# Kernel tuning notes

Measured on AMD Instinct MI355X. Metric: run time of the kernel, lower is better.

Reference implementation:

```python
import jax, jax.numpy as jnp
import numpy as np
from jax import lax

N, F, V = 16, 5, 4  # batch, frames, nodes-per-frame

def _maxpool3(x):
    # MaxPool2d(kernel=3, stride=3), NCHW
    return lax.reduce_window(x, -jnp.inf, lax.max, (1, 1, 3, 3), (1, 1, 3, 3), 'VALID')

def _conv(x, w, b):
    y = lax.conv_general_dilated(x, w, window_strides=(2, 2), padding='VALID',
                                 dimension_numbers=('NCHW', 'OIHW', 'NCHW'))
    return y + b[None, :, None, None]

def setup_inputs() -> dict:
    key = jax.random.key(0)
    ks = jax.random.split(key, 24)
    s = 0.05
    inp = {
        'nodes':  jax.random.normal(ks[0], (N, F, V, 3, 224, 224), jnp.float32),
        'pos':    jax.random.normal(ks[1], (N, F, V, 6), jnp.float32),
        'attmap': jax.random.uniform(ks[2], (N, F, V, V), jnp.float32),
        'depths': jax.random.normal(ks[3], (N, F, V), jnp.float32),
        # params (linear weights stored [in, out]; y = x @ W + b)
        'conv1_w': jax.random.normal(ks[4], (3, 3, 3, 3), jnp.float32) * s,
        'conv1_b': jax.random.normal(ks[5], (3,), jnp.float32) * s,
        'conv2_w': jax.random.normal(ks[6], (1, 3, 3, 3), jnp.float32) * s,
        'conv2_b': jax.random.normal(ks[7], (1,), jnp.float32) * s,
        'lin_w':   jax.random.normal(ks[8], (36, 6), jnp.float32) * s,
        'lin_b':   jax.random.normal(ks[9], (6,), jnp.float32) * s,
        'wfc_w':   jax.random.normal(ks[10], (24, 1), jnp.float32) * s,
        'wfc_b':   jax.random.normal(ks[11], (1,), jnp.float32) * s,
        'fm_w':    jax.random.normal(ks[12], (6, 6), jnp.float32) * s,
        'fm_b':    jax.random.normal(ks[13], (6,), jnp.float32) * s,
        'lm_w':    jax.random.normal(ks[14], (6, 6), jnp.float32) * s,
        'lm_b':    jax.random.normal(ks[15], (6,), jnp.float32) * s,
        'fc1_w':   jax.random.normal(ks[16], (240, 120), jnp.float32) * s,
        'fc1_b':   jax.random.normal(ks[17], (120,), jnp.float32) * s,
        'fc2_w':   jax.random.normal(ks[18], (120, 60), jnp.float32) * s,
        'fc2_b':   jax.random.normal(ks[19], (60,), jnp.float32) * s,
        'fc3_w':   jax.random.normal(ks[20], (60, 6), jnp.float32) * s,
        'fc3_b':   jax.random.normal(ks[21], (6,), jnp.float32) * s,
    }
    return inp

def reference(nodes, pos, attmap, depths,
              conv1_w, conv1_b, conv2_w, conv2_b, lin_w, lin_b,
              wfc_w, wfc_b, fm_w, fm_b, lm_w, lm_b,
              fc1_w, fc1_b, fc2_w, fc2_b, fc3_w, fc3_b):
    # --- CNN node encoder ---
    x = nodes.reshape(N * F * V, 3, 224, 224)
    h = jax.nn.relu(_maxpool3(_conv(x, conv1_w, conv1_b)))          # [B*,3,37,37]
    h = jax.nn.relu(_maxpool3(_conv(h, conv2_w, conv2_b)))          # [B*,1,6,6]
    feat = h.reshape(N, F, V, 36) @ lin_w + lin_b                    # [N,F,V,6]

    # --- edge weights: sigmoid(W . cat(feat_src, feat_tgt)) ---
    na = jnp.concatenate([feat, pos], axis=-1)                       # [N,F,V,12]
    src = jnp.broadcast_to(na[:, :, :, None, :], (N, F, V, V, 12))   # s along axis 2
    tgt = jnp.broadcast_to(na[:, :, None, :, :], (N, F, V, V, 12))   # t along axis 3
    ef = jnp.concatenate([src, tgt], axis=-1)                        # [N,F,V,V,24]
    link = jax.nn.sigmoid((ef @ wfc_w)[..., 0] + wfc_b[0])           # [N,F,s,t]

    maw = link + attmap                                              # [N,F,s,t]

    # --- attention-weighted message aggregation over source nodes ---
    pm = pos @ fm_w + fm_b                                           # [N,F,V,6]
    agg = jnp.einsum('bfsn,bfsd->bfnd', maw, pm)                     # [N,F,V,6]

    # last-frame message (frame 0 has none)
    prev = jnp.concatenate([jnp.zeros_like(pos[:, :1]), pos[:, :-1]], axis=1)
    lm = prev @ lm_w + lm_b                                          # [N,F,V,6]
    frame_mask = (jnp.arange(F) > 0)[None, :, None, None]
    pos_up = agg + jnp.where(frame_mask, lm, 0.0)

    # --- readout MLP ---
    inp = jnp.concatenate([feat, pos_up], axis=-1).reshape(N, F * V * 12)  # [N,240]
    r = jax.nn.relu(inp @ fc1_w + fc1_b)
    r = jax.nn.relu(r @ fc2_w + fc2_b)
    return r @ fc3_w + fc3_b                                         # [N,6]
```

## Files before the change

### kernel.cpp

```cpp
#include <hip/hip_runtime.h>
#include <math.h>

#define NB 16
#define NF 5
#define NV 4
#define NIMG (NB*NF*NV)
#define IMG_HW 224
#define IMG_CH_STRIDE (224*224)
#define H1_HW 37
#define H1_CH_STRIDE (37*37)
#define H1_IMG 4108

__global__ __launch_bounds__(256) void k1_conv1_pool(
    const float* __restrict__ nodes,
    const float* __restrict__ w,
    const float* __restrict__ bias,
    float* __restrict__ h1)
{
    const int blk = blockIdx.x;
    const int img = blk / H1_HW;
    const int py  = blk - img * H1_HW;
    const int t   = threadIdx.x;

    __shared__ float s[3 * 7 * 224];

    const float* src = nodes + (size_t)img * 3 * IMG_CH_STRIDE + py * 6 * IMG_HW;

    {
        const float4* s0 = (const float4*)(src);
        const float4* s1 = (const float4*)(src + IMG_CH_STRIDE);
        const float4* s2 = (const float4*)(src + 2 * IMG_CH_STRIDE);
        float4* d0 = (float4*)s;
        float4* d1 = (float4*)(s + 1568);
        float4* d2 = (float4*)(s + 3136);
        const bool hi = (t < 392 - 256);
        float4 a0 = s0[t], a1 = s1[t], a2 = s2[t];
        float4 b0, b1, b2;
        if (hi) { b0 = s0[t + 256]; b1 = s1[t + 256]; b2 = s2[t + 256]; }
        d0[t] = a0; d1[t] = a1; d2[t] = a2;
        if (hi) { d0[t + 256] = b0; d1[t + 256] = b1; d2[t + 256] = b2; }
    }
    __syncthreads();

    if (t < H1_HW) {
        const int px = t;
        float acc[3][9];
        #pragma unroll
        for (int oc = 0; oc < 3; ++oc)
            #pragma unroll
            for (int p = 0; p < 9; ++p) acc[oc][p] = 0.f;

        #pragma unroll
        for (int ic = 0; ic < 3; ++ic) {
            float wv[3][3][3];
            #pragma unroll
            for (int oc = 0; oc < 3; ++oc)
                #pragma unroll
                for (int ky = 0; ky < 3; ++ky)
                    #pragma unroll
                    for (int kx = 0; kx < 3; ++kx)
                        wv[oc][ky][kx] = w[((oc * 3 + ic) * 3 + ky) * 3 + kx];

            float patch[7][8];
            #pragma unroll
            for (int r = 0; r < 7; ++r) {
                const float* row = s + ic * 1568 + r * 224 + 6 * px;
                #pragma unroll
                for (int k = 0; k < 4; ++k) {
                    float2 q = *(const float2*)(row + 2 * k);
                    patch[r][2 * k]     = q.x;
                    patch[r][2 * k + 1] = q.y;
                }
            }

            #pragma unroll
            for (int i = 0; i < 3; ++i)
                #pragma unroll
                for (int j = 0; j < 3; ++j) {
                    const int p = i * 3 + j;
                    #pragma unroll
                    for (int ky = 0; ky < 3; ++ky)
                        #pragma unroll
                        for (int kx = 0; kx < 3; ++kx) {
                            float x = patch[2 * i + ky][2 * j + kx];
                            acc[0][p] += wv[0][ky][kx] * x;
                            acc[1][p] += wv[1][ky][kx] * x;
                            acc[2][p] += wv[2][ky][kx] * x;
                        }
                }
        }

        float* outb = h1 + (size_t)img * H1_IMG + py * H1_HW + px;
        #pragma unroll
        for (int oc = 0; oc < 3; ++oc) {
            float m = -INFINITY;
            #pragma unroll
            for (int p = 0; p < 9; ++p) m = fmaxf(m, acc[oc][p]);
            m += bias[oc];
            m = fmaxf(m, 0.f);
            outb[oc * H1_CH_STRIDE] = m;
        }
    }
}

__global__ __launch_bounds__(128) void k2_conv2_pool_lin(
    const float* __restrict__ h1,
    const float* __restrict__ w2,
    const float* __restrict__ b2,
    const float* __restrict__ lin_w,
    const float* __restrict__ lin_b,
    float* __restrict__ feat)
{
    const int img = blockIdx.x;
    const int t   = threadIdx.x;
    __shared__ float s[H1_IMG];
    __shared__ float s_h2[36];

    {
        const float4* src = (const float4*)(h1 + (size_t)img * H1_IMG);
        float4* d = (float4*)s;
        float4 v[8];
        #pragma unroll
        for (int k = 0; k < 8; ++k) v[k] = src[t + 128 * k];
        const bool hi = (t < 1027 - 1024);
        float4 v8;
        if (hi) v8 = src[t + 1024];
        #pragma unroll
        for (int k = 0; k < 8; ++k) d[t + 128 * k] = v[k];
        if (hi) d[t + 1024] = v8;
    }
    __syncthreads();

    if (t < 36) {
        const int py = t / 6, px = t - (t / 6) * 6;
        float m = -INFINITY;
        #pragma unroll
        for (int i = 0; i < 3; ++i)
            #pragma unroll
            for (int j = 0; j < 3; ++j) {
                const int oy = 3 * py + i, ox = 3 * px + j;
                float a = 0.f;
                #pragma unroll
                for (int ic = 0; ic < 3; ++ic)
                    #pragma unroll
                    for (int ky = 0; ky < 3; ++ky)
                        #pragma unroll
                        for (int kx = 0; kx < 3; ++kx)
                            a += w2[(ic * 3 + ky) * 3 + kx] *
                                 s[ic * H1_CH_STRIDE + (2 * oy + ky) * H1_HW + (2 * ox + kx)];
                m = fmaxf(m, a);
            }
        m += b2[0];
        s_h2[t] = fmaxf(m, 0.f);
    }
    __syncthreads();
    if (t < 6) {
        float a = lin_b[t];
        #pragma unroll
        for (int i = 0; i < 36; ++i) a += s_h2[i] * lin_w[i * 6 + t];
        feat[img * 6 + t] = a;
    }
}

__global__ __launch_bounds__(128) void k3_graph_mlp(
    const float* __restrict__ feat,
    const float* __restrict__ pos,
    const float* __restrict__ attmap,
    const float* __restrict__ wfc_w,
    const float* __restrict__ wfc_b,
    const float* __restrict__ fm_w,
    const float* __restrict__ fm_b,
    const float* __restrict__ lm_w,
    const float* __restrict__ lm_b,
    const float* __restrict__ fc1_w,
    const float* __restrict__ fc1_b,
    const float* __restrict__ fc2_w,
    const float* __restrict__ fc2_b,
    const float* __restrict__ fc3_w,
    const float* __restrict__ fc3_b,
    float* __restrict__ out)
{
    const int b = blockIdx.x;
    const int t = threadIdx.x;

    __shared__ float s_na[NF][NV][12];
    __shared__ float s_pm[NF][NV][6];
    __shared__ float s_maw[NF][NV][NV];
    __shared__ float s_inp[240];
    __shared__ float s_r1[120];
    __shared__ float s_r2[60];

    if (t < 120) {
        int f = t / 24;
        int v = (t / 6) % 4;
        int d = t % 6;
        float fv = feat[((b * NF + f) * NV + v) * 6 + d];
        float pv = pos[((b * NF + f) * NV + v) * 6 + d];
        s_na[f][v][d]     = fv;
        s_na[f][v][6 + d] = pv;
        s_inp[(f * NV + v) * 12 + d] = fv;
    }
    __syncthreads();

    if (t < 120) {
        int f = t / 24;
        int v = (t / 6) % 4;
        int d = t % 6;
        float a = fm_b[d];
        #pragma unroll
        for (int k = 0; k < 6; ++k) a += s_na[f][v][6 + k] * fm_w[k * 6 + d];
        s_pm[f][v][d] = a;
    }
    if (t < 80) {
        int f = t / 16;
        int sidx = (t / 4) % 4;
        int tt = t % 4;
        float x = wfc_b[0];
        #pragma unroll
        for (int k = 0; k < 12; ++k)
            x += wfc_w[k] * s_na[f][sidx][k] + wfc_w[12 + k] * s_na[f][tt][k];
        float sig = 1.f / (1.f + expf(-x));
        s_maw[f][sidx][tt] = sig + attmap[((b * NF + f) * NV + sidx) * NV + tt];
    }
    __syncthreads();

    if (t < 120) {
        int f = t / 24;
        int n = (t / 6) % 4;
        int d = t % 6;
        float a = 0.f;
        #pragma unroll
        for (int sidx = 0; sidx < 4; ++sidx) a += s_maw[f][sidx][n] * s_pm[f][sidx][d];
        if (f > 0) {
            float l = lm_b[d];
            #pragma unroll
            for (int k = 0; k < 6; ++k) l += s_na[f - 1][n][6 + k] * lm_w[k * 6 + d];
            a += l;
        }
        s_inp[(f * NV + n) * 12 + 6 + d] = a;
    }
    __syncthreads();

    if (t < 120) {
        float a = fc1_b[t];
        #pragma unroll 16
        for (int i = 0; i < 240; ++i) a += s_inp[i] * fc1_w[i * 120 + t];
        s_r1[t] = fmaxf(a, 0.f);
    }
    __syncthreads();

    if (t < 60) {
        float a = fc2_b[t];
        #pragma unroll 16
        for (int i = 0; i < 120; ++i) a += s_r1[i] * fc2_w[i * 60 + t];
        s_r2[t] = fmaxf(a, 0.f);
    }
    __syncthreads();

    if (t < 6) {
        float a = fc3_b[t];
        #pragma unroll 12
        for (int i = 0; i < 60; ++i) a += s_r2[i] * fc3_w[i * 6 + t];
        out[b * 6 + t] = a;
    }
}

extern "C" void kernel_launch(void* const* d_in, const int* in_sizes, int n_in,
                              void* d_out, int out_size, void* d_ws, size_t ws_size,
                              hipStream_t stream) {
    const float* nodes   = (const float*)d_in[0];
    const float* pos     = (const float*)d_in[1];
    const float* attmap  = (const float*)d_in[2];
    const float* conv1_w = (const float*)d_in[4];
    const float* conv1_b = (const float*)d_in[5];
    const float* conv2_w = (const float*)d_in[6];
    const float* conv2_b = (const float*)d_in[7];
    const float* lin_w   = (const float*)d_in[8];
    const float* lin_b   = (const float*)d_in[9];
    const float* wfc_w   = (const float*)d_in[10];
    const float* wfc_b   = (const float*)d_in[11];
    const float* fm_w    = (const float*)d_in[12];
    const float* fm_b    = (const float*)d_in[13];
    const float* lm_w    = (const float*)d_in[14];
    const float* lm_b    = (const float*)d_in[15];
    const float* fc1_w   = (const float*)d_in[16];
    const float* fc1_b   = (const float*)d_in[17];
    const float* fc2_w   = (const float*)d_in[18];
    const float* fc2_b   = (const float*)d_in[19];
    const float* fc3_w   = (const float*)d_in[20];
    const float* fc3_b   = (const float*)d_in[21];

    float* h1      = (float*)d_ws;
    float* feat_ws = h1 + (size_t)NIMG * H1_IMG;

    k1_conv1_pool<<<NIMG * H1_HW, 256, 0, stream>>>(nodes, conv1_w, conv1_b, h1);
    k2_conv2_pool_lin<<<NIMG, 128, 0, stream>>>(h1, conv2_w, conv2_b, lin_w, lin_b, feat_ws);
    k3_graph_mlp<<<NB, 128, 0, stream>>>(feat_ws, pos, attmap,
                                         wfc_w, wfc_b, fm_w, fm_b, lm_w, lm_b,
                                         fc1_w, fc1_b, fc2_w, fc2_b, fc3_w, fc3_b,
                                         (float*)d_out);
}
```

Baseline: 328.8 us.

## Process two pooled rows per block and split output channels across threads

Each conv1+pool block now handles two pooled output rows, loading 13 input rows into shared memory instead of 7. This shares the overlapping halo row and halves the number of blocks. Work is spread so each of up to 222 threads computes one output channel for one pixel, instead of 37 threads computing all three channels, which raises active lanes per block. Weights and bias are staged in shared memory, and the input loads use nontemporal hints. In exchange the blocks use more LDS, and each patch is read from shared memory three times, once per channel thread.

After: 321.2 us (median of 2 runs). 1.02x faster.

```diff
diff --git a/kernel.cpp b/kernel.cpp
--- a/kernel.cpp
+++ b/kernel.cpp
@@ -10,6 +10,9 @@
 #define H1_HW 37
 #define H1_CH_STRIDE (37*37)
 #define H1_IMG 4108
+#define PB_PER_IMG 19
+
+typedef float v4f __attribute__((ext_vector_type(4)));
 
 __global__ __launch_bounds__(256) void k1_conv1_pool(
     const float* __restrict__ nodes,
@@ -18,58 +21,64 @@
     float* __restrict__ h1)
 {
     const int blk = blockIdx.x;
-    const int img = blk / H1_HW;
-    const int py  = blk - img * H1_HW;
+    const int img = blk / PB_PER_IMG;
+    const int pb  = blk - img * PB_PER_IMG;
     const int t   = threadIdx.x;
 
-    __shared__ float s[3 * 7 * 224];
-
-    const float* src = nodes + (size_t)img * 3 * IMG_CH_STRIDE + py * 6 * IMG_HW;
+    const int py0    = 2 * pb;
+    const int nrows  = (pb == PB_PER_IMG - 1) ? 1 : 2;
+    const int r0     = 12 * pb;
+    const int nflt   = (6 * nrows + 1) * 224;
+    const int nf4    = nflt >> 2;
+
+    __shared__ float s[3 * 13 * 224];
+    __shared__ float s_w[27 * 3];
+    __shared__ float s_b[3];
+
+    if (t < 81) s_w[t] = w[t];
+    if (t < 3)  s_b[t] = bias[t];
 
     {
-        const float4* s0 = (const float4*)(src);
-        const float4* s1 = (const float4*)(src + IMG_CH_STRIDE);
-        const float4* s2 = (const float4*)(src + 2 * IMG_CH_STRIDE);
-        float4* d0 = (float4*)s;
-        float4* d1 = (float4*)(s + 1568);
-        float4* d2 = (float4*)(s + 3136);
-        const bool hi = (t < 392 - 256);
-        float4 a0 = s0[t], a1 = s1[t], a2 = s2[t];
-        float4 b0, b1, b2;
-        if (hi) { b0 = s0[t + 256]; b1 = s1[t + 256]; b2 = s2[t + 256]; }
-        d0[t] = a0; d1[t] = a1; d2[t] = a2;
-        if (hi) { d0[t + 256] = b0; d1[t + 256] = b1; d2[t + 256] = b2; }
-    }
-    __syncthreads();
-
-    if (t < H1_HW) {
-        const int px = t;
-        float acc[3][9];
-        #pragma unroll
-        for (int oc = 0; oc < 3; ++oc)
-            #pragma unroll
-            for (int p = 0; p < 9; ++p) acc[oc][p] = 0.f;
+        const v4f* s0 = (const v4f*)(nodes + (size_t)img * 3 * IMG_CH_STRIDE + r0 * IMG_HW);
+        const v4f* s1 = s0 + (IMG_CH_STRIDE >> 2);
+        const v4f* s2 = s1 + (IMG_CH_STRIDE >> 2);
+        v4f* d0 = (v4f*)s;
+        v4f* d1 = (v4f*)(s + nflt);
+        v4f* d2 = (v4f*)(s + 2 * nflt);
+        for (int i = t; i < nf4; i += 256) {
+            v4f a0 = __builtin_nontemporal_load(&s0[i]);
+            v4f a1 = __builtin_nontemporal_load(&s1[i]);
+            v4f a2 = __builtin_nontemporal_load(&s2[i]);
+            d0[i] = a0; d1[i] = a1; d2[i] = a2;
+        }
+    }
+    __syncthreads();
+
+    if (t < 111 * nrows) {
+        const int r  = (t >= 111) ? 1 : 0;
+        const int u  = t - 111 * r;
+        const int oc = u / 37;
+        const int px = u - 37 * oc;
+
+        float acc[9];
+        #pragma unroll
+        for (int p = 0; p < 9; ++p) acc[p] = 0.f;
 
         #pragma unroll
         for (int ic = 0; ic < 3; ++ic) {
-            float wv[3][3][3];
-            #pragma unroll
-            for (int oc = 0; oc < 3; ++oc)
-                #pragma unroll
-                for (int ky = 0; ky < 3; ++ky)
-                    #pragma unroll
-                    for (int kx = 0; kx < 3; ++kx)
-                        wv[oc][ky][kx] = w[((oc * 3 + ic) * 3 + ky) * 3 + kx];
+            float wv[9];
+            #pragma unroll
+            for (int k = 0; k < 9; ++k) wv[k] = s_w[(oc * 3 + ic) * 9 + k];
 
             float patch[7][8];
             #pragma unroll
-            for (int r = 0; r < 7; ++r) {
-                const float* row = s + ic * 1568 + r * 224 + 6 * px;
+            for (int rr = 0; rr < 7; ++rr) {
+                const float* row = s + ic * nflt + (6 * r + rr) * 224 + 6 * px;
                 #pragma unroll
                 for (int k = 0; k < 4; ++k) {
                     float2 q = *(const float2*)(row + 2 * k);
-                    patch[r][2 * k]     = q.x;
-                    patch[r][2 * k + 1] = q.y;
+                    patch[rr][2 * k]     = q.x;
+                    patch[rr][2 * k + 1] = q.y;
                 }
             }
 
@@ -81,25 +90,17 @@
                     #pragma unroll
                     for (int ky = 0; ky < 3; ++ky)
                         #pragma unroll
-                        for (int kx = 0; kx < 3; ++kx) {
-                            float x = patch[2 * i + ky][2 * j + kx];
-                            acc[0][p] += wv[0][ky][kx] * x;
-                            acc[1][p] += wv[1][ky][kx] * x;
-                            acc[2][p] += wv[2][ky][kx] * x;
-                        }
+                        for (int kx = 0; kx < 3; ++kx)
+                            acc[p] += wv[ky * 3 + kx] * patch[2 * i + ky][2 * j + kx];
                 }
         }
 
-        float* outb = h1 + (size_t)img * H1_IMG + py * H1_HW + px;
-        #pragma unroll
-        for (int oc = 0; oc < 3; ++oc) {
-            float m = -INFINITY;
-            #pragma unroll
-            for (int p = 0; p < 9; ++p) m = fmaxf(m, acc[oc][p]);
-            m += bias[oc];
-            m = fmaxf(m, 0.f);
-            outb[oc * H1_CH_STRIDE] = m;
-        }
+        float m = -INFINITY;
+        #pragma unroll
+        for (int p = 0; p < 9; ++p) m = fmaxf(m, acc[p]);
+        m += s_b[oc];
+        m = fmaxf(m, 0.f);
+        h1[(size_t)img * H1_IMG + oc * H1_CH_STRIDE + (py0 + r) * H1_HW + px] = m;
     }
 }
 
@@ -293,7 +294,7 @@
     float* h1      = (float*)d_ws;
     float* feat_ws = h1 + (size_t)NIMG * H1_IMG;
 
-    k1_conv1_pool<<<NIMG * H1_HW, 256, 0, stream>>>(nodes, conv1_w, conv1_b, h1);
+    k1_conv1_pool<<<NIMG * PB_PER_IMG, 256, 0, stream>>>(nodes, conv1_w, conv1_b, h1);
     k2_conv2_pool_lin<<<NIMG, 128, 0, stream>>>(h1, conv2_w, conv2_b, lin_w, lin_b, feat_ws);
     k3_graph_mlp<<<NB, 128, 0, stream>>>(feat_ws, pos, attmap,
                                          wfc_w, wfc_b, fm_w, fm_b, lm_w, lm_b,
```

## Process three pooled rows per block and load tiles with global_load_lds

Applied to the files above, without the earlier changes.

Each conv1+pool block now covers three pooled output rows (19 input rows), so the halo row shared between adjacent row-groups is loaded once instead of twice and 111 of 256 threads compute instead of 37. The shared-memory fill uses direct global-to-LDS loads, which bypass registers. In exchange, per-block LDS rises to about 51KB, lowering occupancy, and the grid shrinks to 13 blocks per image with a shorter final block.

Measured after the change: 329.6 us. About the same (+0.2%).

```diff
diff --git a/kernel.cpp b/kernel.cpp
--- a/kernel.cpp
+++ b/kernel.cpp
@@ -10,6 +10,7 @@
 #define H1_HW 37
 #define H1_CH_STRIDE (37*37)
 #define H1_IMG 4108
+#define PB_PER_IMG 13
 
 __global__ __launch_bounds__(256) void k1_conv1_pool(
     const float* __restrict__ nodes,
@@ -18,32 +19,42 @@
     float* __restrict__ h1)
 {
     const int blk = blockIdx.x;
-    const int img = blk / H1_HW;
-    const int py  = blk - img * H1_HW;
+    const int img = blk / PB_PER_IMG;
+    const int pb  = blk - img * PB_PER_IMG;
     const int t   = threadIdx.x;
 
-    __shared__ float s[3 * 7 * 224];
-
-    const float* src = nodes + (size_t)img * 3 * IMG_CH_STRIDE + py * 6 * IMG_HW;
+    const int last   = (pb == PB_PER_IMG - 1);
+    const int py0    = 3 * pb;
+    const int nrows  = last ? 1 : 3;
+    const int r0     = 18 * pb;
+    const int nflt   = (6 * nrows + 1) * 224;
+    const int nf4    = nflt >> 2;
+
+    __shared__ float s[3 * 19 * 224];
 
     {
-        const float4* s0 = (const float4*)(src);
-        const float4* s1 = (const float4*)(src + IMG_CH_STRIDE);
-        const float4* s2 = (const float4*)(src + 2 * IMG_CH_STRIDE);
-        float4* d0 = (float4*)s;
-        float4* d1 = (float4*)(s + 1568);
-        float4* d2 = (float4*)(s + 3136);
-        const bool hi = (t < 392 - 256);
-        float4 a0 = s0[t], a1 = s1[t], a2 = s2[t];
-        float4 b0, b1, b2;
-        if (hi) { b0 = s0[t + 256]; b1 = s1[t + 256]; b2 = s2[t + 256]; }
-        d0[t] = a0; d1[t] = a1; d2[t] = a2;
-        if (hi) { d0[t + 256] = b0; d1[t + 256] = b1; d2[t + 256] = b2; }
-    }
-    __syncthreads();
-
-    if (t < H1_HW) {
-        const int px = t;
+        const float* g0 = nodes + (size_t)img * 3 * IMG_CH_STRIDE + r0 * IMG_HW;
+        const float* g1 = g0 + IMG_CH_STRIDE;
+        const float* g2 = g0 + 2 * IMG_CH_STRIDE;
+        for (int i = t; i < nf4; i += 256) {
+            const int o = 4 * i;
+            __builtin_amdgcn_global_load_lds(
+                (const __attribute__((address_space(1))) unsigned int*)(g0 + o),
+                (__attribute__((address_space(3))) unsigned int*)(s + o), 16, 0, 0);
+            __builtin_amdgcn_global_load_lds(
+                (const __attribute__((address_space(1))) unsigned int*)(g1 + o),
+                (__attribute__((address_space(3))) unsigned int*)(s + nflt + o), 16, 0, 0);
+            __builtin_amdgcn_global_load_lds(
+                (const __attribute__((address_space(1))) unsigned int*)(g2 + o),
+                (__attribute__((address_space(3))) unsigned int*)(s + 2 * nflt + o), 16, 0, 0);
+        }
+    }
+    __syncthreads();
+
+    if (t < H1_HW * nrows) {
+        const int r  = t / H1_HW;
+        const int px = t - H1_HW * r;
+
         float acc[3][9];
         #pragma unroll
         for (int oc = 0; oc < 3; ++oc)
@@ -52,24 +63,22 @@
 
         #pragma unroll
         for (int ic = 0; ic < 3; ++ic) {
-            float wv[3][3][3];
+            float wv[3][9];
             #pragma unroll
             for (int oc = 0; oc < 3; ++oc)
                 #pragma unroll
-                for (int ky = 0; ky < 3; ++ky)
-                    #pragma unroll
-                    for (int kx = 0; kx < 3; ++kx)
-                        wv[oc][ky][kx] = w[((oc * 3 + ic) * 3 + ky) * 3 + kx];
+                for (int k = 0; k < 9; ++k)
+                    wv[oc][k] = w[(oc * 3 + ic) * 9 + k];
 
             float patch[7][8];
             #pragma unroll
-            for (int r = 0; r < 7; ++r) {
-                const float* row = s + ic * 1568 + r * 224 + 6 * px;
+            for (int rr = 0; rr < 7; ++rr) {
+                const float* row = s + ic * nflt + (6 * r + rr) * 224 + 6 * px;
                 #pragma unroll
                 for (int k = 0; k < 4; ++k) {
                     float2 q = *(const float2*)(row + 2 * k);
-                    patch[r][2 * k]     = q.x;
-                    patch[r][2 * k + 1] = q.y;
+                    patch[rr][2 * k]     = q.x;
+                    patch[rr][2 * k + 1] = q.y;
                 }
             }
 
@@ -83,14 +92,14 @@
                         #pragma unroll
                         for (int kx = 0; kx < 3; ++kx) {
                             float x = patch[2 * i + ky][2 * j + kx];
-                            acc[0][p] += wv[0][ky][kx] * x;
-                            acc[1][p] += wv[1][ky][kx] * x;
-                            acc[2][p] += wv[2][ky][kx] * x;
+                            acc[0][p] += wv[0][ky * 3 + kx] * x;
+                            acc[1][p] += wv[1][ky * 3 + kx] * x;
+                            acc[2][p] += wv[2][ky * 3 + kx] * x;
                         }
                 }
         }
 
-        float* outb = h1 + (size_t)img * H1_IMG + py * H1_HW + px;
+        float* outb = h1 + (size_t)img * H1_IMG + (py0 + r) * H1_HW + px;
         #pragma unroll
         for (int oc = 0; oc < 3; ++oc) {
             float m = -INFINITY;
@@ -293,7 +302,7 @@
     float* h1      = (float*)d_ws;
     float* feat_ws = h1 + (size_t)NIMG * H1_IMG;
 
-    k1_conv1_pool<<<NIMG * H1_HW, 256, 0, stream>>>(nodes, conv1_w, conv1_b, h1);
+    k1_conv1_pool<<<NIMG * PB_PER_IMG, 256, 0, stream>>>(nodes, conv1_w, conv1_b, h1);
     k2_conv2_pool_lin<<<NIMG, 128, 0, stream>>>(h1, conv2_w, conv2_b, lin_w, lin_b, feat_ws);
     k3_graph_mlp<<<NB, 128, 0, stream>>>(feat_ws, pos, attmap,
                                          wfc_w, wfc_b, fm_w, fm_b, lm_w, lm_b,
```
